# Kernel optimization log

Measured on AMD Instinct MI355X. Metric: run time of the kernel, lower is better.

## Reference

```python
import jax, jax.numpy as jnp
import numpy as np

MAX_SOURCE_LEN = 2048
HIDDEN = 1024
HEADS = 16
NUM_BUCKETS = 32
MAX_DISTANCE = 128
LN_EPS = 1e-5


def relative_position_bucket(relative_position, num_buckets=NUM_BUCKETS, max_distance=MAX_DISTANCE):
    # Bidirectional T5-style bucketing.
    n = -relative_position
    half = num_buckets // 2
    ret = (n < 0).astype(jnp.int32) * half
    n = jnp.abs(n)
    max_exact = half // 2
    is_small = n < max_exact
    scale = (half - max_exact) / np.log(max_distance / max_exact)
    val_large = max_exact + (jnp.log(jnp.maximum(n, 1).astype(jnp.float32) / max_exact) * scale).astype(jnp.int32)
    val_large = jnp.minimum(val_large, half - 1)
    return ret + jnp.where(is_small, n.astype(jnp.int32), val_large)


def setup_inputs() -> dict:
    key = jax.random.key(0)
    ks = jax.random.split(key, 6)
    B, L = 4, 1024
    leaf_idx = jax.random.randint(ks[0], (B, L), 0, MAX_SOURCE_LEN)
    p_emb = jax.random.normal(ks[1], (MAX_SOURCE_LEN, HIDDEN), jnp.float32) * 0.02
    p_emb = p_emb.at[0].set(0.0)  # padding_idx=0
    r_emb = jax.random.normal(ks[2], (NUM_BUCKETS + 1, HEADS), jnp.float32) * 0.02
    r_emb = r_emb.at[NUM_BUCKETS].set(0.0)  # padding_idx=num_buckets
    Wq = jax.random.normal(ks[3], (HIDDEN, HIDDEN), jnp.float32) / np.sqrt(HIDDEN)
    Wk = jax.random.normal(ks[4], (HIDDEN, HIDDEN), jnp.float32) / np.sqrt(HIDDEN)
    return {
        "leaf_idx": leaf_idx,
        "p_emb": p_emb,
        "r_emb": r_emb,
        "ln_g": jnp.ones((HIDDEN,), jnp.float32),
        "ln_b": jnp.zeros((HIDDEN,), jnp.float32),
        "Wq": Wq,
        "bq": jnp.zeros((HIDDEN,), jnp.float32),
        "Wk": Wk,
        "bk": jnp.zeros((HIDDEN,), jnp.float32),
    }


def reference(leaf_idx, p_emb, r_emb, ln_g, ln_b, Wq, bq, Wk, bk):
    B, L = leaf_idx.shape
    H = r_emb.shape[1]
    d_k = p_emb.shape[1] // H

    # --- T5 relative-position bias ---
    # rel[b,i,j] = leaf[b,j] - leaf[b,i]  (matches unsqueeze(1) - unsqueeze(-1))
    rel = leaf_idx[:, None, :] - leaf_idx[:, :, None]
    bucket = relative_position_bucket(rel)
    valid = leaf_idx != 0
    pair = valid[:, None, :] & valid[:, :, None]
    bucket = jnp.where(pair, bucket, NUM_BUCKETS)
    t5_score = jnp.transpose(r_emb[bucket], (0, 3, 1, 2))  # [B,H,L,L]

    # --- untied position score ---
    x = p_emb[leaf_idx]  # [B,L,D]
    mu = jnp.mean(x, axis=-1, keepdims=True)
    var = jnp.mean(jnp.square(x - mu), axis=-1, keepdims=True)
    xn = (x - mu) * jax.lax.rsqrt(var + LN_EPS) * ln_g + ln_b

    q = (xn @ Wq.T + bq).reshape(B, L, H, d_k).transpose(0, 2, 1, 3) / np.sqrt(d_k)
    k = (xn @ Wk.T + bk).reshape(B, L, H, d_k).transpose(0, 2, 1, 3)
    untied = jnp.einsum("bhid,bhjd->bhij", q, k)

    return untied + t5_score  # leaf_PE_Type == 'Merge'
```

## Files before the change

### kernel.cpp

```cpp
#include <hip/hip_runtime.h>
#include <hip/hip_bf16.h>

typedef __attribute__((ext_vector_type(8))) short short8;
typedef __attribute__((ext_vector_type(4))) float f32x4;

#define L 1024
#define D 1024
#define NHEADS 16

static __device__ __forceinline__ unsigned short f2bf(float f) {
  union { float f; unsigned int u; } c; c.f = f;
  unsigned int u = c.u;
  u += 0x7fffu + ((u >> 16) & 1u);
  return (unsigned short)(u >> 16);
}

static __device__ __forceinline__ void gload_lds16(const void* gsrc, void* ldst) {
  __builtin_amdgcn_global_load_lds(
      (const __attribute__((address_space(1))) void*)gsrc,
      (__attribute__((address_space(3))) void*)ldst, 16, 0, 0);
}

__global__ __launch_bounds__(256) void prep_kernel(const int* __restrict__ leaf,
                                                   const float* __restrict__ p_emb,
                                                   const float* __restrict__ g,
                                                   const float* __restrict__ bcoef,
                                                   const float* __restrict__ Wq,
                                                   const float* __restrict__ Wk,
                                                   unsigned short* __restrict__ w,
                                                   unsigned short* __restrict__ xn) {
  int bid = blockIdx.x;
  int t = threadIdx.x;
  if (bid < 2048) {
    int idx = bid * 256 + t;
    bool isq = (idx < 262144);
    const float* src = isq ? Wq : Wk;
    float sc = isq ? 0.125f : 1.0f;
    int rel = isq ? idx : idx - 262144;
    float4 v = ((const float4*)src)[rel];
    ushort4 o;
    o.x = f2bf(v.x * sc); o.y = f2bf(v.y * sc); o.z = f2bf(v.z * sc); o.w = f2bf(v.w * sc);
    ((ushort4*)w)[idx] = o;
  } else {
    int row = bid - 2048;
    int lane = t & 63, wv = t >> 6;
    int leafv = leaf[row];
    float4 xv = ((const float4*)(p_emb + (size_t)leafv * D))[t];
    float s  = xv.x + xv.y + xv.z + xv.w;
    float s2 = xv.x*xv.x + xv.y*xv.y + xv.z*xv.z + xv.w*xv.w;
    #pragma unroll
    for (int o = 1; o < 64; o <<= 1) {
      s  += __shfl_xor(s, o);
      s2 += __shfl_xor(s2, o);
    }
    __shared__ float red[8];
    if (lane == 0) { red[wv*2] = s; red[wv*2+1] = s2; }
    __syncthreads();
    float st  = red[0] + red[2] + red[4] + red[6];
    float s2t = red[1] + red[3] + red[5] + red[7];
    float mu = st * (1.0f/1024.0f);
    float var = s2t * (1.0f/1024.0f) - mu*mu;
    float rs = rsqrtf(var + 1e-5f);
    float4 gv = ((const float4*)g)[t];
    float4 bv = ((const float4*)bcoef)[t];
    ushort4 o;
    o.x = f2bf((xv.x - mu) * rs * gv.x + bv.x);
    o.y = f2bf((xv.y - mu) * rs * gv.y + bv.y);
    o.z = f2bf((xv.z - mu) * rs * gv.z + bv.z);
    o.w = f2bf((xv.w - mu) * rs * gv.w + bv.w);
    ((ushort4*)xn)[row * 256 + t] = o;
  }
}

__global__ __launch_bounds__(256) void qk_bucket_kernel(const unsigned short* __restrict__ xn,
                                                        const unsigned short* __restrict__ wqk,
                                                        const float* __restrict__ bq,
                                                        const float* __restrict__ bk,
                                                        const int* __restrict__ leaf,
                                                        unsigned short* __restrict__ qws,
                                                        unsigned short* __restrict__ kws,
                                                        unsigned char* __restrict__ bucket) {
  __shared__ __align__(16) unsigned short As[2][128 * 32];
  __shared__ __align__(16) unsigned short Bs[2][64 * 32];
  int bid = blockIdx.x;
  int t = threadIdx.x;

  if (bid >= 1024) {
    int idx = (bid - 1024) * 256 + t;
    int j = idx & 1023;
    int rest = idx >> 10;
    int i = rest & 1023;
    int b = rest >> 10;
    int li = leaf[b * L + i];
    int lj = leaf[b * L + j];
    int n = li - lj;
    int ret = 0;
    if (n < 0) { ret = 16; n = -n; }
    int val;
    if (n < 8) {
      val = n;
    } else {
      val = 8 + (int)(logf((float)n * 0.125f) * 2.8853900817779268f);
      if (val > 15) val = 15;
    }
    val += ret;
    if (li == 0 || lj == 0) val = 32;
    bucket[idx] = (unsigned char)val;
    return;
  }

  int lane = t & 63, w = t >> 6;
  int wr = w >> 1, wc = w & 1;
  int swz = (bid & 7) * 128 + (bid >> 3);
  int m0 = (swz >> 5) * 128;
  int n0 = (swz & 31) * 64;

  f32x4 acc[4][2] = {};

  auto stage = [&](int buf, int kt) {
    int k0 = kt * 32;
    #pragma unroll
    for (int r = 0; r < 2; ++r) {
      int c = t + r * 256;
      int row = c >> 2, kc = c & 3;
      gload_lds16(xn + (size_t)(m0 + row) * D + k0 + kc * 8, &As[buf][c * 8]);
    }
    {
      int row = t >> 2, kc = t & 3;
      gload_lds16(wqk + (size_t)(n0 + row) * D + k0 + kc * 8, &Bs[buf][t * 8]);
    }
  };

  stage(0, 0);
  __syncthreads();
  for (int kt = 0; kt < 32; ++kt) {
    int cur = kt & 1;
    if (kt < 31) stage(cur ^ 1, kt + 1);
    short8 a[4], b[2];
    #pragma unroll
    for (int f = 0; f < 4; ++f) {
      int arow = wr * 64 + f * 16 + (lane & 15);
      a[f] = *(const short8*)&As[cur][arow * 32 + (lane >> 4) * 8];
    }
    #pragma unroll
    for (int f = 0; f < 2; ++f) {
      int brow = wc * 32 + f * 16 + (lane & 15);
      b[f] = *(const short8*)&Bs[cur][brow * 32 + (lane >> 4) * 8];
    }
    __builtin_amdgcn_s_setprio(1);
    #pragma unroll
    for (int i = 0; i < 4; ++i)
      #pragma unroll
      for (int j = 0; j < 2; ++j)
        acc[i][j] = __builtin_amdgcn_mfma_f32_16x16x32_bf16(b[j], a[i], acc[i][j], 0, 0, 0);
    __builtin_amdgcn_s_setprio(0);
    __syncthreads();
  }

  bool isq = (n0 < 1024);
  const float* bias = isq ? bq : bk;
  float scale = isq ? 0.125f : 1.0f;
  unsigned short* outp = isq ? qws : kws;
  int nbase = n0 - (isq ? 0 : 1024);

  float4 bv[2];
  #pragma unroll
  for (int j = 0; j < 2; ++j) {
    bv[j] = *(const float4*)(bias + nbase + wc * 32 + j * 16 + (lane >> 4) * 4);
    bv[j].x *= scale; bv[j].y *= scale; bv[j].z *= scale; bv[j].w *= scale;
  }

  #pragma unroll
  for (int i = 0; i < 4; ++i) {
    int m = m0 + wr * 64 + i * 16 + (lane & 15);
    int bb = m >> 10, ii = m & 1023;
    #pragma unroll
    for (int j = 0; j < 2; ++j) {
      int n0c = nbase + wc * 32 + j * 16 + (lane >> 4) * 4;
      int h = n0c >> 6, k0 = n0c & 63;
      int bh = bb * NHEADS + h;
      unsigned p0 = (unsigned)f2bf(acc[i][j][0] + bv[j].x) | ((unsigned)f2bf(acc[i][j][1] + bv[j].y) << 16);
      unsigned p1 = (unsigned)f2bf(acc[i][j][2] + bv[j].z) | ((unsigned)f2bf(acc[i][j][3] + bv[j].w) << 16);
      size_t off = (size_t)bh * 65536 + (size_t)(ii >> 4) * 1024
                 + (size_t)(k0 >> 3) * 128 + (ii & 15) * 8 + (k0 & 7);
      uint2 pv; pv.x = p0; pv.y = p1;
      *(uint2*)(outp + off) = pv;
    }
  }
}

__global__ __launch_bounds__(256) void untied_kernel(const unsigned short* __restrict__ qws,
                                                     const unsigned short* __restrict__ kws,
                                                     const unsigned char* __restrict__ bucket,
                                                     const float* __restrict__ r_emb,
                                                     float* __restrict__ out) {
  __shared__ float rt[33 * 17];
  __shared__ __align__(16) unsigned char bt[128 * 128];
  int t = threadIdx.x;
  for (int idx = t; idx < 528; idx += 256)
    rt[(idx >> 4) * 17 + (idx & 15)] = r_emb[idx];

  int bid = blockIdx.x;
  int lg = (bid & 7) * 512 + (bid >> 3);
  int h  = lg & 15;
  int jt = (lg >> 4) & 7;
  int it = (lg >> 7) & 7;
  int b  = lg >> 10;
  int lane = t & 63, w = t >> 6;
  int wr = w >> 1, wc = w & 1;
  int i0 = it * 128, j0 = jt * 128;
  int bh = b * NHEADS + h;

  const unsigned char* bsrc = bucket + (size_t)b * L * L + (size_t)i0 * L + j0;
  {
    #pragma unroll
    for (int iter = 0; iter < 4; ++iter) {
      int lofs = iter * 4096 + w * 1024 + lane * 16;
      int row = lofs >> 7;
      int cb = (lofs >> 4) & 7;
      gload_lds16(bsrc + (size_t)row * L + (size_t)((cb ^ (row & 7)) << 4), &bt[lofs]);
    }
  }

  const unsigned short* qb = qws + (size_t)bh * 65536;
  const unsigned short* kb = kws + (size_t)bh * 65536;

  short8 a[4][2], bf[4][2];
  #pragma unroll
  for (int f = 0; f < 4; ++f) {
    #pragma unroll
    for (int ks = 0; ks < 2; ++ks) {
      a[f][ks]  = *(const short8*)(qb + (size_t)(i0 / 16 + wr * 4 + f) * 1024 + ks * 512 + lane * 8);
      bf[f][ks] = *(const short8*)(kb + (size_t)(j0 / 16 + wc * 4 + f) * 1024 + ks * 512 + lane * 8);
    }
  }

  __syncthreads();

  f32x4 acc[4][4] = {};
  #pragma unroll
  for (int ks = 0; ks < 2; ++ks)
    #pragma unroll
    for (int i = 0; i < 4; ++i)
      #pragma unroll
      for (int j = 0; j < 4; ++j)
        acc[i][j] = __builtin_amdgcn_mfma_f32_16x16x32_bf16(bf[j][ks], a[i][ks], acc[i][j], 0, 0, 0);

  unsigned bw[4][4];
  #pragma unroll
  for (int i = 0; i < 4; ++i) {
    int il = wr * 64 + i * 16 + (lane & 15);
    #pragma unroll
    for (int j = 0; j < 4; ++j) {
      int jl = wc * 64 + j * 16 + (lane >> 4) * 4;
      int jd = jl >> 2;
      int addr = il * 128 + (((jd >> 2) ^ (il & 7)) << 4) + ((jd & 3) << 2);
      bw[i][j] = *(const unsigned*)&bt[addr];
    }
  }

  float* ob = out + (size_t)bh * L * L;
  const float* rth = rt + h;
  #pragma unroll
  for (int i = 0; i < 4; ++i) {
    int il = wr * 64 + i * 16 + (lane & 15);
    #pragma unroll
    for (int j = 0; j < 4; ++j) {
      int jl = wc * 64 + j * 16 + (lane >> 4) * 4;
      unsigned w32 = bw[i][j];
      float4 o;
      o.x = acc[i][j][0] + rth[(w32 & 255u) * 17];
      o.y = acc[i][j][1] + rth[((w32 >> 8) & 255u) * 17];
      o.z = acc[i][j][2] + rth[((w32 >> 16) & 255u) * 17];
      o.w = acc[i][j][3] + rth[(w32 >> 24) * 17];
      *(float4*)(ob + (size_t)(i0 + il) * L + (j0 + jl)) = o;
    }
  }
}

extern "C" void kernel_launch(void* const* d_in, const int* in_sizes, int n_in,
                              void* d_out, int out_size, void* d_ws, size_t ws_size,
                              hipStream_t stream) {
  const int*   leaf  = (const int*)d_in[0];
  const float* p_emb = (const float*)d_in[1];
  const float* r_emb = (const float*)d_in[2];
  const float* ln_g  = (const float*)d_in[3];
  const float* ln_b  = (const float*)d_in[4];
  const float* Wq    = (const float*)d_in[5];
  const float* bq    = (const float*)d_in[6];
  const float* Wk    = (const float*)d_in[7];
  const float* bk    = (const float*)d_in[8];
  float* out = (float*)d_out;

  char* ws = (char*)d_ws;
  unsigned short* xn   = (unsigned short*)(ws);
  unsigned short* wqk  = (unsigned short*)(ws + (8u  << 20));
  unsigned short* qws  = (unsigned short*)(ws + (12u << 20));
  unsigned short* kws  = (unsigned short*)(ws + (20u << 20));
  unsigned char*  bckt = (unsigned char*)(ws + (28u << 20));

  prep_kernel<<<6144, 256, 0, stream>>>(leaf, p_emb, ln_g, ln_b, Wq, Wk, wqk, xn);
  qk_bucket_kernel<<<17408, 256, 0, stream>>>(xn, wqk, bq, bk, leaf, qws, kws, bckt);
  untied_kernel<<<4096, 256, 0, stream>>>(qws, kws, bckt, r_emb, out);
}
```

Baseline: 106.8 us.

## Use per-wave LayerNorm rows, drop setprio, and store output nontemporally

The LayerNorm part of the prep kernel now gives each wavefront one whole row instead of one row per block. That removes the shared-memory reduction and the block barrier, and the prep grid shrinks to match. The s_setprio hints around the MFMA loop in the QK GEMM are removed. The final output stores in the untied kernel become nontemporal, to avoid polluting the cache with the large write-only score tensor.

```diff
diff --git a/kernel.cpp b/kernel.cpp
--- a/kernel.cpp
+++ b/kernel.cpp
@@ -42,33 +42,40 @@
     o.x = f2bf(v.x * sc); o.y = f2bf(v.y * sc); o.z = f2bf(v.z * sc); o.w = f2bf(v.w * sc);
     ((ushort4*)w)[idx] = o;
   } else {
-    int row = bid - 2048;
     int lane = t & 63, wv = t >> 6;
+    int row = (bid - 2048) * 4 + wv;
     int leafv = leaf[row];
-    float4 xv = ((const float4*)(p_emb + (size_t)leafv * D))[t];
-    float s  = xv.x + xv.y + xv.z + xv.w;
-    float s2 = xv.x*xv.x + xv.y*xv.y + xv.z*xv.z + xv.w*xv.w;
+    const float4* src = (const float4*)(p_emb + (size_t)leafv * D);
+    float4 xv[4];
+    #pragma unroll
+    for (int r = 0; r < 4; ++r) xv[r] = src[lane + r * 64];
+    float s = 0.f, s2 = 0.f;
+    #pragma unroll
+    for (int r = 0; r < 4; ++r) {
+      s  += xv[r].x + xv[r].y + xv[r].z + xv[r].w;
+      s2 += xv[r].x*xv[r].x + xv[r].y*xv[r].y + xv[r].z*xv[r].z + xv[r].w*xv[r].w;
+    }
     #pragma unroll
     for (int o = 1; o < 64; o <<= 1) {
       s  += __shfl_xor(s, o);
       s2 += __shfl_xor(s2, o);
     }
-    __shared__ float red[8];
-    if (lane == 0) { red[wv*2] = s; red[wv*2+1] = s2; }
-    __syncthreads();
-    float st  = red[0] + red[2] + red[4] + red[6];
-    float s2t = red[1] + red[3] + red[5] + red[7];
-    float mu = st * (1.0f/1024.0f);
-    float var = s2t * (1.0f/1024.0f) - mu*mu;
+    float mu = s * (1.0f/1024.0f);
+    float var = s2 * (1.0f/1024.0f) - mu*mu;
     float rs = rsqrtf(var + 1e-5f);
-    float4 gv = ((const float4*)g)[t];
-    float4 bv = ((const float4*)bcoef)[t];
-    ushort4 o;
-    o.x = f2bf((xv.x - mu) * rs * gv.x + bv.x);
-    o.y = f2bf((xv.y - mu) * rs * gv.y + bv.y);
-    o.z = f2bf((xv.z - mu) * rs * gv.z + bv.z);
-    o.w = f2bf((xv.w - mu) * rs * gv.w + bv.w);
-    ((ushort4*)xn)[row * 256 + t] = o;
+    const float4* gp = (const float4*)g;
+    const float4* bp = (const float4*)bcoef;
+    #pragma unroll
+    for (int r = 0; r < 4; ++r) {
+      float4 gv = gp[lane + r * 64];
+      float4 bv = bp[lane + r * 64];
+      ushort4 o;
+      o.x = f2bf((xv[r].x - mu) * rs * gv.x + bv.x);
+      o.y = f2bf((xv[r].y - mu) * rs * gv.y + bv.y);
+      o.z = f2bf((xv[r].z - mu) * rs * gv.z + bv.z);
+      o.w = f2bf((xv[r].w - mu) * rs * gv.w + bv.w);
+      ((ushort4*)xn)[row * 256 + lane + r * 64] = o;
+    }
   }
 }
 
@@ -147,13 +154,11 @@
       int brow = wc * 32 + f * 16 + (lane & 15);
       b[f] = *(const short8*)&Bs[cur][brow * 32 + (lane >> 4) * 8];
     }
-    __builtin_amdgcn_s_setprio(1);
     #pragma unroll
     for (int i = 0; i < 4; ++i)
       #pragma unroll
       for (int j = 0; j < 2; ++j)
         acc[i][j] = __builtin_amdgcn_mfma_f32_16x16x32_bf16(b[j], a[i], acc[i][j], 0, 0, 0);
-    __builtin_amdgcn_s_setprio(0);
     __syncthreads();
   }
 
@@ -268,12 +273,12 @@
     for (int j = 0; j < 4; ++j) {
       int jl = wc * 64 + j * 16 + (lane >> 4) * 4;
       unsigned w32 = bw[i][j];
-      float4 o;
-      o.x = acc[i][j][0] + rth[(w32 & 255u) * 17];
-      o.y = acc[i][j][1] + rth[((w32 >> 8) & 255u) * 17];
-      o.z = acc[i][j][2] + rth[((w32 >> 16) & 255u) * 17];
-      o.w = acc[i][j][3] + rth[(w32 >> 24) * 17];
-      *(float4*)(ob + (size_t)(i0 + il) * L + (j0 + jl)) = o;
+      f32x4 o = acc[i][j];
+      o[0] += rth[(w32 & 255u) * 17];
+      o[1] += rth[((w32 >> 8) & 255u) * 17];
+      o[2] += rth[((w32 >> 16) & 255u) * 17];
+      o[3] += rth[(w32 >> 24) * 17];
+      __builtin_nontemporal_store(o, (f32x4*)(ob + (size_t)(i0 + il) * L + (j0 + jl)));
     }
   }
 }
@@ -299,7 +304,7 @@
   unsigned short* kws  = (unsigned short*)(ws + (20u << 20));
   unsigned char*  bckt = (unsigned char*)(ws + (28u << 20));
 
-  prep_kernel<<<6144, 256, 0, stream>>>(leaf, p_emb, ln_g, ln_b, Wq, Wk, wqk, xn);
+  prep_kernel<<<3072, 256, 0, stream>>>(leaf, p_emb, ln_g, ln_b, Wq, Wk, wqk, xn);
   qk_bucket_kernel<<<17408, 256, 0, stream>>>(xn, wqk, bq, bk, leaf, qws, kws, bckt);
   untied_kernel<<<4096, 256, 0, stream>>>(qws, kws, bckt, r_emb, out);
 }
```

Result: slower. 133.8 us (+25.3%).
